# Kernel tuning notes

Hardware: AMD Instinct MI355X
Metric: run time of the kernel (lower is better)

The kernel has to match this reference:

```python
import jax, jax.numpy as jnp
import numpy as np
from jax import lax

B, C, H, W = 8, 384, 64, 64


def cos_map(N):
    # ortho DCT-II basis: weight[n, x] = cos(n*(x+0.5)*pi/N) * sqrt(2/N), row 0 /= sqrt(2)
    wx = (jnp.arange(N, dtype=jnp.float32) + 0.5) / N
    wn = jnp.arange(N, dtype=jnp.float32)[:, None]
    w = jnp.cos(wn * wx[None, :] * jnp.pi) * np.sqrt(2.0 / N).astype(np.float32)
    return w.at[0, :].multiply(np.float32(1.0 / np.sqrt(2.0)))


def setup_inputs() -> dict:
    key = jax.random.key(0)
    ks = jax.random.split(key, 8)
    s = 0.05
    return {
        "x": jax.random.normal(ks[0], (B, C, H, W), jnp.float32),
        "freq_embed": jax.random.normal(ks[1], (H, W, C), jnp.float32),
        "dw_w": jax.random.normal(ks[2], (C, 1, 3, 3), jnp.float32) * s,
        "dw_b": jnp.zeros((C,), jnp.float32),
        "lin_w": jax.random.normal(ks[3], (2 * C, C), jnp.float32) * s,
        "lin_b": jnp.zeros((2 * C,), jnp.float32),
        "tok_w": jax.random.normal(ks[4], (C, C), jnp.float32) * s,
        "tok_b": jnp.zeros((C,), jnp.float32),
        "c": jnp.ones((1,), jnp.float32),
        "alpha": jnp.ones((1,), jnp.float32) * 0.1,
        "ln_g": jnp.ones((C,), jnp.float32),
        "ln_b": jnp.zeros((C,), jnp.float32),
        "out_w": jax.random.normal(ks[5], (C, C), jnp.float32) * s,
        "out_b": jnp.zeros((C,), jnp.float32),
    }


def reference(x, freq_embed, dw_w, dw_b, lin_w, lin_b, tok_w, tok_b, c, alpha, ln_g, ln_b, out_w, out_b):
    Bc, Cc, Hc, Wc = x.shape
    # depthwise 3x3 conv
    x = lax.conv_general_dilated(x, dw_w, (1, 1), 'SAME',
                                 feature_group_count=Cc,
                                 dimension_numbers=('NCHW', 'OIHW', 'NCHW'))
    x = x + dw_b[None, :, None, None]
    # linear to 2C (channels-last), split into signal x and gate z
    xz = jnp.einsum('bchw,dc->bhwd', x, lin_w) + lin_b
    xs, z = xz[..., :Cc], xz[..., Cc:]          # [B,H,W,C]
    xs = jnp.transpose(xs, (0, 3, 1, 2))        # [B,C,H,W]
    # 2D ortho DCT-II: D = Wh @ x @ Ww^T
    Wh, Ww = cos_map(Hc), cos_map(Wc)
    Xd = jnp.einsum('nh,bchw,kw->bcnk', Wh, xs, Ww)
    # learned frequency gating: t = ReLU(Linear(freq_embed)), per (H,W,C)
    t = jax.nn.relu(jnp.einsum('hwc,dc->hwd', freq_embed, tok_w) + tok_b)
    ct = jnp.transpose(jnp.cos(c * t), (2, 0, 1))[None]        # [1,C,H,W]
    st = jnp.transpose(jnp.sin(c * t), (2, 0, 1))[None] / c[0]
    # x_u0 == x_v0 == Xd in the original (dct2d applied twice to same x)
    final = ct * Xd + st * (Xd + 0.5 * alpha[0] * Xd)
    # 2D inverse DCT: x = Wh^T @ D @ Ww
    xi = jnp.einsum('nh,bcnk,kw->bchw', Wh, final, Ww)
    # LayerNorm over channels, gate with SiLU(z), output linear
    y = jnp.transpose(xi, (0, 2, 3, 1))          # [B,H,W,C]
    mu = jnp.mean(y, axis=-1, keepdims=True)
    var = jnp.mean((y - mu) ** 2, axis=-1, keepdims=True)
    y = (y - mu) * lax.rsqrt(var + 1e-5) * ln_g + ln_b
    y = y * jax.nn.silu(z)
    y = jnp.einsum('bhwc,dc->bhwd', y, out_w) + out_b
    return jnp.transpose(y, (0, 3, 1, 2))        # [B,C,H,W]
```

## Files before the change

kernel.cpp:

```cpp
#include <hip/hip_runtime.h>

typedef _Float16 h2 __attribute__((ext_vector_type(2)));
typedef _Float16 h4 __attribute__((ext_vector_type(4)));
typedef _Float16 h8 __attribute__((ext_vector_type(8)));
typedef float    f4 __attribute__((ext_vector_type(4)));

#define MFMA32(a,b,c) __builtin_amdgcn_mfma_f32_16x16x32_f16((a),(b),(c),0,0,0)
#define MFMA16(a,b,c) __builtin_amdgcn_mfma_f32_16x16x16f16((a),(b),(c),0,0,0)

#define B_N 8
#define C_N 384
#define P_N 4096
#define PI_F 3.14159265358979323846f

__device__ __forceinline__ h4 to_h4(f4 v) {
  h4 r; r[0]=(_Float16)v[0]; r[1]=(_Float16)v[1]; r[2]=(_Float16)v[2]; r[3]=(_Float16)v[3];
  return r;
}

__global__ __launch_bounds__(256) void k_setup(
    const float* __restrict__ lin_w, const float* __restrict__ tok_w,
    const float* __restrict__ out_w, _Float16* __restrict__ lwh,
    _Float16* __restrict__ twh, _Float16* __restrict__ owh,
    _Float16* __restrict__ wmg, _Float16* __restrict__ wmtg) {
  int t = blockIdx.x * 256 + threadIdx.x;
  if (t < 768*384) lwh[t] = (_Float16)lin_w[t];
  if (t < 384*384) { twh[t] = (_Float16)tok_w[t]; owh[t] = (_Float16)out_w[t]; }
  if (t < 4096) {
    int n = t >> 6, h = t & 63;
    float v = cosf((float)n * ((float)h + 0.5f) * (PI_F / 64.0f)) * 0.1767766952966369f;
    if (n == 0) v *= 0.7071067811865476f;
    wmg[n*64 + h]  = (_Float16)v;
    wmtg[h*64 + n] = (_Float16)v;
  }
}

__global__ __launch_bounds__(256) void k_dwconv(
    const float* __restrict__ x, const float* __restrict__ dww,
    const float* __restrict__ dwb, _Float16* __restrict__ xdw) {
  int blk = blockIdx.x;
  int h = blk & 63;
  int rest = blk >> 6;
  int cgi = rest % 6;
  int b = rest / 6;
  int c0 = cgi * 64;
  int t = threadIdx.x;
  int w = t & 63, ci = t >> 6;
  __shared__ _Float16 buf[64 * 68];
  const float* xb = x + (size_t)b * C_N * P_N;
  int wl = (w > 0)  ? w - 1 : 0;
  int wr = (w < 63) ? w + 1 : 63;
  #pragma unroll
  for (int j = 0; j < 8; j++) {
    int lc = ci * 16 + j * 2;
    h2 pr;
    #pragma unroll
    for (int e = 0; e < 2; e++) {
      int c = c0 + lc + e;
      const float* xc = xb + (size_t)c * P_N;
      float k0=dww[c*9+0],k1=dww[c*9+1],k2=dww[c*9+2];
      float k3=dww[c*9+3],k4=dww[c*9+4],k5=dww[c*9+5];
      float k6=dww[c*9+6],k7=dww[c*9+7],k8=dww[c*9+8];
      float top = (h > 0)  ? xc[(h-1)*64 + w] : 0.0f;
      float mid = xc[h*64 + w];
      float bot = (h < 63) ? xc[(h+1)*64 + w] : 0.0f;
      float tl = __shfl(top, wl, 64), tr = __shfl(top, wr, 64);
      float ml = __shfl(mid, wl, 64), mr = __shfl(mid, wr, 64);
      float bl = __shfl(bot, wl, 64), br = __shfl(bot, wr, 64);
      if (w == 0)  { tl = 0.f; ml = 0.f; bl = 0.f; }
      if (w == 63) { tr = 0.f; mr = 0.f; br = 0.f; }
      float acc = dwb[c];
      acc += k0*tl + k1*top + k2*tr;
      acc += k3*ml + k4*mid + k5*mr;
      acc += k6*bl + k7*bot + k8*br;
      pr[e] = (_Float16)acc;
    }
    *(h2*)&buf[w*68 + lc] = pr;
  }
  __syncthreads();
  _Float16* op = xdw + ((size_t)b*P_N + h*64) * C_N + c0;
  #pragma unroll
  for (int i = 0; i < 4; i++) {
    int flat = (t + 256*i) * 4;
    int pix = flat >> 6, cl = flat & 63;
    *(h4*)&op[(size_t)pix*C_N + cl] = *(const h4*)&buf[pix*68 + cl];
  }
}

__global__ __launch_bounds__(256) void k_gate(
    const float* __restrict__ fe, const _Float16* __restrict__ twh,
    const float* __restrict__ tkb, const float* __restrict__ cc,
    const float* __restrict__ aa, _Float16* __restrict__ g) {
  int pt = blockIdx.x & 63, dt = blockIdx.x >> 6;
  int p0 = pt*64, d0 = dt*64;
  int t = threadIdx.x, lane = t & 63, wave = t >> 6;
  int quad = lane >> 4, l15 = lane & 15;
  int wm_ = wave >> 1, wn = wave & 1;
  __shared__ _Float16 la[64*40], lb[64*40];
  int srow = t >> 2, scg = (t & 3) * 8;
  f4 acc[2][2] = {};
  for (int kc = 0; kc < 384; kc += 32) {
    const float* src = fe + (size_t)(p0 + srow)*384 + kc + scg;
    f4 v0 = *(const f4*)src;
    f4 v1 = *(const f4*)(src + 4);
    h8 hv;
    hv[0]=(_Float16)v0[0]; hv[1]=(_Float16)v0[1]; hv[2]=(_Float16)v0[2]; hv[3]=(_Float16)v0[3];
    hv[4]=(_Float16)v1[0]; hv[5]=(_Float16)v1[1]; hv[6]=(_Float16)v1[2]; hv[7]=(_Float16)v1[3];
    *(h8*)&la[srow*40 + scg] = hv;
    *(h8*)&lb[srow*40 + scg] = *(const h8*)&twh[(size_t)(d0 + srow)*384 + kc + scg];
    __syncthreads();
    h8 a0 = *(const h8*)&la[(wm_*32 + l15)*40 + quad*8];
    h8 a1 = *(const h8*)&la[(wm_*32 + 16 + l15)*40 + quad*8];
    h8 b0 = *(const h8*)&lb[(wn*32 + l15)*40 + quad*8];
    h8 b1 = *(const h8*)&lb[(wn*32 + 16 + l15)*40 + quad*8];
    acc[0][0] = MFMA32(a0, b0, acc[0][0]);
    acc[0][1] = MFMA32(a0, b1, acc[0][1]);
    acc[1][0] = MFMA32(a1, b0, acc[1][0]);
    acc[1][1] = MFMA32(a1, b1, acc[1][1]);
    __syncthreads();
  }
  float c0 = cc[0];
  float s1 = (1.0f + 0.5f*aa[0]) / c0;
  #pragma unroll
  for (int i = 0; i < 2; i++)
  #pragma unroll
  for (int j = 0; j < 2; j++) {
    int d  = d0 + wn*32 + j*16 + l15;
    int pl = wm_*32 + i*16 + quad*4;
    float bias = tkb[d];
    h4 hv;
    #pragma unroll
    for (int r = 0; r < 4; r++) {
      float tv = fmaxf(acc[i][j][r] + bias, 0.0f);
      hv[r] = (_Float16)(__cosf(c0*tv) + s1*__sinf(c0*tv));
    }
    *(h4*)&g[(size_t)d*P_N + p0 + pl] = hv;
  }
}

__global__ __launch_bounds__(256) void k_gemm1(
    const _Float16* __restrict__ xdw, const _Float16* __restrict__ lwh,
    const float* __restrict__ lnb, _Float16* __restrict__ xs,
    _Float16* __restrict__ zs) {
  int pt = blockIdx.x & 31;
  int rest = blockIdx.x >> 5;
  int dt = rest % 12, b = rest / 12;
  int p0 = pt * 128, d0 = dt * 64;
  int t = threadIdx.x, lane = t & 63, wave = t >> 6;
  int quad = lane >> 4, l15 = lane & 15;
  __shared__ _Float16 lbs[64 * 392];
  {
    int row = t >> 2, cb = (t & 3) * 8;
    const _Float16* gB = lwh + (size_t)(d0 + row) * 384;
    #pragma unroll
    for (int i = 0; i < 12; i++)
      *(h8*)&lbs[row*392 + cb + i*32] = *(const h8*)&gB[cb + i*32];
  }
  __syncthreads();
  const _Float16* pa = xdw + ((size_t)b*P_N + p0 + wave*32 + l15) * 384 + quad*8;
  f4 acc[2][4] = {};
  #pragma unroll
  for (int kc = 0; kc < 384; kc += 32) {
    h8 a0 = *(const h8*)(pa + kc);
    h8 a1 = *(const h8*)(pa + 16*384 + kc);
    h8 bf[4];
    #pragma unroll
    for (int j = 0; j < 4; j++)
      bf[j] = *(const h8*)&lbs[(j*16 + l15)*392 + kc + quad*8];
    #pragma unroll
    for (int j = 0; j < 4; j++) {
      acc[0][j] = MFMA32(a0, bf[j], acc[0][j]);
      acc[1][j] = MFMA32(a1, bf[j], acc[1][j]);
    }
  }
  bool isz = (d0 >= 384);
  #pragma unroll
  for (int j = 0; j < 4; j++) {
    int d = d0 + j*16 + l15;
    float bias = lnb[d];
    _Float16* dst = isz ? (zs + ((size_t)b*C_N + (d-384)) * P_N)
                        : (xs + ((size_t)b*C_N + d) * P_N);
    #pragma unroll
    for (int i = 0; i < 2; i++) {
      int p = p0 + wave*32 + i*16 + quad*4;
      h4 hv;
      if (isz) {
        #pragma unroll
        for (int r = 0; r < 4; r++) {
          float v = acc[i][j][r] + bias;
          v = v / (1.0f + __expf(-v));
          hv[r] = (_Float16)v;
        }
      } else {
        #pragma unroll
        for (int r = 0; r < 4; r++) hv[r] = (_Float16)(acc[i][j][r] + bias);
      }
      *(h4*)&dst[p] = hv;
    }
  }
}

__global__ __launch_bounds__(256) void k_dct(
    const _Float16* __restrict__ xs, const _Float16* __restrict__ g,
    const _Float16* __restrict__ wmg, const _Float16* __restrict__ wmtg,
    _Float16* __restrict__ xi) {
  int b = blockIdx.x / 96, cg = blockIdx.x % 96;
  int c0 = cg * 4;
  int t = threadIdx.x, wave = t >> 6, lane = t & 63;
  int quad = lane >> 4, l15 = lane & 15;
  __shared__ _Float16 wm_s[64*72];
  __shared__ _Float16 wmt_s[64*72];
  __shared__ _Float16 pb[4][64*72];
  for (int i = t; i < 512; i += 256) {
    int row = i >> 3, col = (i & 7) * 8;
    *(h8*)&wm_s[row*72 + col]  = *(const h8*)&wmg[row*64 + col];
    *(h8*)&wmt_s[row*72 + col] = *(const h8*)&wmtg[row*64 + col];
  }
  const _Float16* xsb = xs + ((size_t)b*C_N + c0) * P_N;
  for (int i = t; i < 2048; i += 256) {
    int pl = i >> 9, idx = i & 511;
    int p = idx * 8, hh = p >> 6, ww = p & 63;
    *(h8*)&pb[pl][hh*72 + ww] = *(const h8*)&xsb[(size_t)pl*P_N + p];
  }
  __syncthreads();
  h8 aS[4][2], bW[4][2];
  #pragma unroll
  for (int I = 0; I < 4; I++)
  #pragma unroll
  for (int kk = 0; kk < 2; kk++) {
    aS[I][kk] = *(const h8*)&pb[wave][(I*16 + l15)*72 + kk*32 + quad*8];
    bW[I][kk] = *(const h8*)&wm_s[(I*16 + l15)*72 + kk*32 + quad*8];
  }
  h4 t1h[4][4];
  #pragma unroll
  for (int I = 0; I < 4; I++)
  #pragma unroll
  for (int J = 0; J < 4; J++) {
    f4 a = {};
    a = MFMA32(aS[I][0], bW[J][0], a);
    a = MFMA32(aS[I][1], bW[J][1], a);
    t1h[I][J] = to_h4(a);
  }
  __syncthreads();
  const _Float16* gb = g + (size_t)c0 * P_N;
  for (int i = t; i < 2048; i += 256) {
    int pl = i >> 9, idx = i & 511;
    int p = idx * 8, hh = p >> 6, ww = p & 63;
    *(h8*)&pb[pl][hh*72 + ww] = *(const h8*)&gb[(size_t)pl*P_N + p];
  }
  __syncthreads();
  f4 t2[4][4] = {};
  #pragma unroll
  for (int I = 0; I < 4; I++)
  #pragma unroll
  for (int K4 = 0; K4 < 4; K4++) {
    h4 af = *(const h4*)&wm_s[(I*16 + l15)*72 + K4*16 + quad*4];
    #pragma unroll
    for (int J = 0; J < 4; J++) t2[I][J] = MFMA16(af, t1h[K4][J], t2[I][J]);
  }
  h4 fh[4][4];
  #pragma unroll
  for (int I = 0; I < 4; I++)
  #pragma unroll
  for (int J = 0; J < 4; J++) {
    int n0 = I*16 + quad*4, k = J*16 + l15;
    h4 r;
    #pragma unroll
    for (int rr = 0; rr < 4; rr++) {
      float gv = (float)pb[wave][(n0+rr)*72 + k];
      r[rr] = (_Float16)(t2[I][J][rr] * gv);
    }
    fh[I][J] = r;
  }
  f4 t3[4][4] = {};
  #pragma unroll
  for (int J = 0; J < 4; J++)
  #pragma unroll
  for (int K4 = 0; K4 < 4; K4++) {
    h4 bf = *(const h4*)&wmt_s[(J*16 + l15)*72 + K4*16 + quad*4];
    #pragma unroll
    for (int I = 0; I < 4; I++) t3[I][J] = MFMA16(fh[K4][I], bf, t3[I][J]);
  }
  h4 t3h[4][4];
  #pragma unroll
  for (int I = 0; I < 4; I++)
  #pragma unroll
  for (int J = 0; J < 4; J++) t3h[I][J] = to_h4(t3[I][J]);
  f4 t4[4][4] = {};
  #pragma unroll
  for (int I = 0; I < 4; I++)
  #pragma unroll
  for (int K4 = 0; K4 < 4; K4++) {
    h4 af = *(const h4*)&wmt_s[(I*16 + l15)*72 + K4*16 + quad*4];
    #pragma unroll
    for (int J = 0; J < 4; J++) t4[I][J] = MFMA16(af, t3h[K4][J], t4[I][J]);
  }
  #pragma unroll
  for (int I = 0; I < 4; I++)
  #pragma unroll
  for (int J = 0; J < 4; J++) {
    int w0 = I*16 + quad*4, hq = J*16 + l15;
    *(h4*)&pb[wave][hq*72 + w0] = to_h4(t4[I][J]);
  }
  __syncthreads();
  _Float16* xib = xi + ((size_t)b*C_N + c0) * P_N;
  for (int i = t; i < 2048; i += 256) {
    int pl = i >> 9, idx = i & 511;
    int p = idx * 8, hh = p >> 6, ww = p & 63;
    *(h8*)&xib[(size_t)pl*P_N + p] = *(const h8*)&pb[pl][hh*72 + ww];
  }
}

__global__ __launch_bounds__(256) void k_ubuild(
    const _Float16* __restrict__ xi, const _Float16* __restrict__ zs,
    const float* __restrict__ lng, const float* __restrict__ lnbv,
    _Float16* __restrict__ u) {
  int b = blockIdx.x >> 6, pt = blockIdx.x & 63;
  int p0 = pt * 64;
  int t = threadIdx.x;
  __shared__ _Float16 ut[64 * 392];
  __shared__ float red[4][64], red2[4][64];
  __shared__ float muL[64], rsL[64];
  int cr = t >> 3;
  int px0 = (t & 7) * 8;
  const _Float16* xib = xi + (size_t)b * C_N * P_N;
  #pragma unroll
  for (int i = 0; i < 12; i++) {
    int c = cr + 32 * i;
    h8 v = *(const h8*)&xib[(size_t)c * P_N + p0 + px0];
    #pragma unroll
    for (int e = 0; e < 8; e++) ut[(px0 + e) * 392 + c] = v[e];
  }
  __syncthreads();
  int px = t & 63, seg = t >> 6;
  float s = 0.f, ss = 0.f;
  #pragma unroll
  for (int j = 0; j < 12; j++) {
    h8 v = *(const h8*)&ut[px * 392 + seg * 96 + j * 8];
    #pragma unroll
    for (int e = 0; e < 8; e++) { float f = (float)v[e]; s += f; ss += f * f; }
  }
  red[seg][px] = s; red2[seg][px] = ss;
  __syncthreads();
  if (t < 64) {
    float st  = red[0][t] + red[1][t] + red[2][t] + red[3][t];
    float sst = red2[0][t] + red2[1][t] + red2[2][t] + red2[3][t];
    float m = st * (1.f/384.f);
    float var = sst * (1.f/384.f) - m * m;
    muL[t] = m; rsL[t] = rsqrtf(var + 1e-5f);
  }
  __syncthreads();
  const _Float16* zb = zs + (size_t)b * C_N * P_N;
  #pragma unroll
  for (int i = 0; i < 12; i++) {
    int c = cr + 32 * i;
    float g = lng[c], bb = lnbv[c];
    h8 zv = *(const h8*)&zb[(size_t)c * P_N + p0 + px0];
    #pragma unroll
    for (int e = 0; e < 8; e++) {
      int p = px0 + e;
      float y = ((float)ut[p * 392 + c] - muL[p]) * rsL[p] * g + bb;
      ut[p * 392 + c] = (_Float16)(y * (float)zv[e]);
    }
  }
  __syncthreads();
  _Float16* ub = u + ((size_t)b * P_N + p0) * C_N;
  #pragma unroll
  for (int i = 0; i < 12; i++) {
    int idx = t + 256 * i;
    int row = idx / 48, ch = idx % 48;
    *(h8*)&ub[(size_t)row * C_N + ch * 8] = *(const h8*)&ut[row * 392 + ch * 8];
  }
}

__global__ __launch_bounds__(256) void k_gemm2(
    const _Float16* __restrict__ u, const _Float16* __restrict__ owh,
    const float* __restrict__ ob, float* __restrict__ out) {
  int pt = blockIdx.x & 31;
  int rest = blockIdx.x >> 5;
  int dt = rest % 6, b = rest / 6;
  int p0 = pt * 128, d0 = dt * 64;
  int t = threadIdx.x, lane = t & 63, wave = t >> 6;
  int quad = lane >> 4, l15 = lane & 15;
  __shared__ _Float16 lbs[64 * 392];
  {
    int row = t >> 2, cb = (t & 3) * 8;
    const _Float16* gB = owh + (size_t)(d0 + row) * 384;
    #pragma unroll
    for (int i = 0; i < 12; i++)
      *(h8*)&lbs[row*392 + cb + i*32] = *(const h8*)&gB[cb + i*32];
  }
  __syncthreads();
  const _Float16* pa = u + ((size_t)b*P_N + p0 + wave*32 + l15) * 384 + quad*8;
  f4 acc[2][4] = {};
  #pragma unroll
  for (int kc = 0; kc < 384; kc += 32) {
    h8 a0 = *(const h8*)(pa + kc);
    h8 a1 = *(const h8*)(pa + 16*384 + kc);
    h8 bf[4];
    #pragma unroll
    for (int j = 0; j < 4; j++)
      bf[j] = *(const h8*)&lbs[(j*16 + l15)*392 + kc + quad*8];
    #pragma unroll
    for (int j = 0; j < 4; j++) {
      acc[0][j] = MFMA32(a0, bf[j], acc[0][j]);
      acc[1][j] = MFMA32(a1, bf[j], acc[1][j]);
    }
  }
  #pragma unroll
  for (int j = 0; j < 4; j++) {
    int d = d0 + j*16 + l15;
    float bias = ob[d];
    #pragma unroll
    for (int i = 0; i < 2; i++) {
      int p = p0 + wave*32 + i*16 + quad*4;
      f4 v;
      #pragma unroll
      for (int r = 0; r < 4; r++) v[r] = acc[i][j][r] + bias;
      *(f4*)&out[((size_t)b*C_N + d)*P_N + p] = v;
    }
  }
}

extern "C" void kernel_launch(void* const* d_in, const int* in_sizes, int n_in,
                              void* d_out, int out_size, void* d_ws, size_t ws_size,
                              hipStream_t stream) {
  (void)in_sizes; (void)n_in; (void)out_size; (void)ws_size;
  const float* x    = (const float*)d_in[0];
  const float* fe   = (const float*)d_in[1];
  const float* dww  = (const float*)d_in[2];
  const float* dwb  = (const float*)d_in[3];
  const float* linw = (const float*)d_in[4];
  const float* linb = (const float*)d_in[5];
  const float* tokw = (const float*)d_in[6];
  const float* tokb = (const float*)d_in[7];
  const float* cc   = (const float*)d_in[8];
  const float* aa   = (const float*)d_in[9];
  const float* lng  = (const float*)d_in[10];
  const float* lnbv = (const float*)d_in[11];
  const float* outw = (const float*)d_in[12];
  const float* outb = (const float*)d_in[13];
  float* out = (float*)d_out;

  char* ws = (char*)d_ws;
  size_t off = 0;
  auto alloc = [&](size_t bytes) -> void* {
    void* p = ws + off;
    off += (bytes + 255) & ~(size_t)255;
    return p;
  };
  _Float16* lwh  = (_Float16*)alloc((size_t)768*384*2);
  _Float16* twh  = (_Float16*)alloc((size_t)384*384*2);
  _Float16* owh  = (_Float16*)alloc((size_t)384*384*2);
  _Float16* wmg  = (_Float16*)alloc((size_t)64*64*2);
  _Float16* wmtg = (_Float16*)alloc((size_t)64*64*2);
  _Float16* xdw  = (_Float16*)alloc((size_t)B_N*P_N*C_N*2);
  _Float16* xs   = (_Float16*)alloc((size_t)B_N*C_N*P_N*2);
  _Float16* zs   = (_Float16*)alloc((size_t)B_N*C_N*P_N*2);
  _Float16* gg   = (_Float16*)alloc((size_t)C_N*P_N*2);
  _Float16* xi   = xdw;
  _Float16* uu   = xs;

  k_setup<<<1152, 256, 0, stream>>>(linw, tokw, outw, lwh, twh, owh, wmg, wmtg);
  k_dwconv<<<3072, 256, 0, stream>>>(x, dww, dwb, xdw);
  k_gate<<<384, 256, 0, stream>>>(fe, twh, tokb, cc, aa, gg);
  k_gemm1<<<3072, 256, 0, stream>>>(xdw, lwh, linb, xs, zs);
  k_dct<<<768, 256, 0, stream>>>(xs, gg, wmg, wmtg, xi);
  k_ubuild<<<512, 256, 0, stream>>>(xi, zs, lng, lnbv, uu);
  k_gemm2<<<1536, 256, 0, stream>>>(uu, owh, outb, out);
}
```

Measured before the change: 270.7 us.

## Enlarge GEMM pixel tiles to 256 and software-pipeline A-fragment loads

In both pointwise GEMM kernels, each block now covers 256 pixels instead of 128, so each wave computes a 64x64 tile with 4x4 accumulators and the LDS-staged weight tile is reused over twice as many rows. Global A-fragment loads are prefetched two K-steps ahead through a small register pipeline to hide memory latency behind MFMA work. Block indexing is reordered so the output-channel tile varies fastest, which lets neighbouring blocks share the same activation rows in cache. The cost is higher register pressure and half as many blocks, which may lower occupancy.

```diff
diff --git a/kernel.cpp b/kernel.cpp
--- a/kernel.cpp
+++ b/kernel.cpp
@@ -142,36 +142,48 @@
     const _Float16* __restrict__ xdw, const _Float16* __restrict__ lwh,
     const float* __restrict__ lnb, _Float16* __restrict__ xs,
     _Float16* __restrict__ zs) {
-  int pt = blockIdx.x & 31;
-  int rest = blockIdx.x >> 5;
-  int dt = rest % 12, b = rest / 12;
-  int p0 = pt * 128, d0 = dt * 64;
+  int blk = blockIdx.x;
+  int dt = blk % 12;
+  int rest = blk / 12;
+  int pt = rest & 15;
+  int b  = rest >> 4;
+  int p0 = pt * 256, d0 = dt * 64;
   int t = threadIdx.x, lane = t & 63, wave = t >> 6;
   int quad = lane >> 4, l15 = lane & 15;
   __shared__ _Float16 lbs[64 * 392];
   {
     int row = t >> 2, cb = (t & 3) * 8;
-    const _Float16* gB = lwh + (size_t)(d0 + row) * 384;
+    const _Float16* gB = lwh + (size_t)(d0 + row) * 384 + cb;
     #pragma unroll
     for (int i = 0; i < 12; i++)
-      *(h8*)&lbs[row*392 + cb + i*32] = *(const h8*)&gB[cb + i*32];
-  }
-  __syncthreads();
-  const _Float16* pa = xdw + ((size_t)b*P_N + p0 + wave*32 + l15) * 384 + quad*8;
-  f4 acc[2][4] = {};
-  #pragma unroll
-  for (int kc = 0; kc < 384; kc += 32) {
-    h8 a0 = *(const h8*)(pa + kc);
-    h8 a1 = *(const h8*)(pa + 16*384 + kc);
+      *(h8*)&lbs[row*392 + cb + i*32] = *(const h8*)&gB[i*32];
+  }
+  __syncthreads();
+  const _Float16* pa = xdw + ((size_t)b*P_N + p0 + wave*64 + l15) * 384 + quad*8;
+  h8 acur[4], anxt[4];
+  #pragma unroll
+  for (int i = 0; i < 4; i++) acur[i] = *(const h8*)(pa + i*16*384);
+  #pragma unroll
+  for (int i = 0; i < 4; i++) anxt[i] = *(const h8*)(pa + i*16*384 + 32);
+  f4 acc[4][4] = {};
+  #pragma unroll
+  for (int it = 0; it < 12; it++) {
+    h8 atmp[4];
+    int kpf = (it < 10) ? (it + 2) * 32 : 0;
+    #pragma unroll
+    for (int i = 0; i < 4; i++) atmp[i] = *(const h8*)(pa + i*16*384 + kpf);
+    int kc = it * 32;
     h8 bf[4];
     #pragma unroll
     for (int j = 0; j < 4; j++)
       bf[j] = *(const h8*)&lbs[(j*16 + l15)*392 + kc + quad*8];
     #pragma unroll
-    for (int j = 0; j < 4; j++) {
-      acc[0][j] = MFMA32(a0, bf[j], acc[0][j]);
-      acc[1][j] = MFMA32(a1, bf[j], acc[1][j]);
-    }
+    for (int i = 0; i < 4; i++)
+    #pragma unroll
+    for (int j = 0; j < 4; j++)
+      acc[i][j] = MFMA32(acur[i], bf[j], acc[i][j]);
+    #pragma unroll
+    for (int i = 0; i < 4; i++) { acur[i] = anxt[i]; anxt[i] = atmp[i]; }
   }
   bool isz = (d0 >= 384);
   #pragma unroll
@@ -181,8 +193,8 @@
     _Float16* dst = isz ? (zs + ((size_t)b*C_N + (d-384)) * P_N)
                         : (xs + ((size_t)b*C_N + d) * P_N);
     #pragma unroll
-    for (int i = 0; i < 2; i++) {
-      int p = p0 + wave*32 + i*16 + quad*4;
+    for (int i = 0; i < 4; i++) {
+      int p = p0 + wave*64 + i*16 + quad*4;
       h4 hv;
       if (isz) {
         #pragma unroll
@@ -376,44 +388,56 @@
 __global__ __launch_bounds__(256) void k_gemm2(
     const _Float16* __restrict__ u, const _Float16* __restrict__ owh,
     const float* __restrict__ ob, float* __restrict__ out) {
-  int pt = blockIdx.x & 31;
-  int rest = blockIdx.x >> 5;
-  int dt = rest % 6, b = rest / 6;
-  int p0 = pt * 128, d0 = dt * 64;
+  int blk = blockIdx.x;
+  int dt = blk % 6;
+  int rest = blk / 6;
+  int pt = rest & 15;
+  int b  = rest >> 4;
+  int p0 = pt * 256, d0 = dt * 64;
   int t = threadIdx.x, lane = t & 63, wave = t >> 6;
   int quad = lane >> 4, l15 = lane & 15;
   __shared__ _Float16 lbs[64 * 392];
   {
     int row = t >> 2, cb = (t & 3) * 8;
-    const _Float16* gB = owh + (size_t)(d0 + row) * 384;
+    const _Float16* gB = owh + (size_t)(d0 + row) * 384 + cb;
     #pragma unroll
     for (int i = 0; i < 12; i++)
-      *(h8*)&lbs[row*392 + cb + i*32] = *(const h8*)&gB[cb + i*32];
-  }
-  __syncthreads();
-  const _Float16* pa = u + ((size_t)b*P_N + p0 + wave*32 + l15) * 384 + quad*8;
-  f4 acc[2][4] = {};
-  #pragma unroll
-  for (int kc = 0; kc < 384; kc += 32) {
-    h8 a0 = *(const h8*)(pa + kc);
-    h8 a1 = *(const h8*)(pa + 16*384 + kc);
+      *(h8*)&lbs[row*392 + cb + i*32] = *(const h8*)&gB[i*32];
+  }
+  __syncthreads();
+  const _Float16* pa = u + ((size_t)b*P_N + p0 + wave*64 + l15) * 384 + quad*8;
+  h8 acur[4], anxt[4];
+  #pragma unroll
+  for (int i = 0; i < 4; i++) acur[i] = *(const h8*)(pa + i*16*384);
+  #pragma unroll
+  for (int i = 0; i < 4; i++) anxt[i] = *(const h8*)(pa + i*16*384 + 32);
+  f4 acc[4][4] = {};
+  #pragma unroll
+  for (int it = 0; it < 12; it++) {
+    h8 atmp[4];
+    int kpf = (it < 10) ? (it + 2) * 32 : 0;
+    #pragma unroll
+    for (int i = 0; i < 4; i++) atmp[i] = *(const h8*)(pa + i*16*384 + kpf);
+    int kc = it * 32;
     h8 bf[4];
     #pragma unroll
     for (int j = 0; j < 4; j++)
       bf[j] = *(const h8*)&lbs[(j*16 + l15)*392 + kc + quad*8];
     #pragma unroll
-    for (int j = 0; j < 4; j++) {
-      acc[0][j] = MFMA32(a0, bf[j], acc[0][j]);
-      acc[1][j] = MFMA32(a1, bf[j], acc[1][j]);
-    }
+    for (int i = 0; i < 4; i++)
+    #pragma unroll
+    for (int j = 0; j < 4; j++)
+      acc[i][j] = MFMA32(acur[i], bf[j], acc[i][j]);
+    #pragma unroll
+    for (int i = 0; i < 4; i++) { acur[i] = anxt[i]; anxt[i] = atmp[i]; }
   }
   #pragma unroll
   for (int j = 0; j < 4; j++) {
     int d = d0 + j*16 + l15;
     float bias = ob[d];
     #pragma unroll
-    for (int i = 0; i < 2; i++) {
-      int p = p0 + wave*32 + i*16 + quad*4;
+    for (int i = 0; i < 4; i++) {
+      int p = p0 + wave*64 + i*16 + quad*4;
       f4 v;
       #pragma unroll
       for (int r = 0; r < 4; r++) v[r] = acc[i][j][r] + bias;
@@ -464,8 +488,8 @@
   k_setup<<<1152, 256, 0, stream>>>(linw, tokw, outw, lwh, twh, owh, wmg, wmtg);
   k_dwconv<<<3072, 256, 0, stream>>>(x, dww, dwb, xdw);
   k_gate<<<384, 256, 0, stream>>>(fe, twh, tokb, cc, aa, gg);
-  k_gemm1<<<3072, 256, 0, stream>>>(xdw, lwh, linb, xs, zs);
+  k_gemm1<<<1536, 256, 0, stream>>>(xdw, lwh, linb, xs, zs);
   k_dct<<<768, 256, 0, stream>>>(xs, gg, wmg, wmtg, xi);
   k_ubuild<<<512, 256, 0, stream>>>(xi, zs, lng, lnbv, uu);
-  k_gemm2<<<1536, 256, 0, stream>>>(uu, owh, outb, out);
-}
+  k_gemm2<<<768, 256, 0, stream>>>(uu, owh, outb, out);
+}
```

Result: slower. 283.4 us (+4.7%).
